# Kernel optimization log

Measured on AMD Instinct MI355X. Metric: run time of the kernel, lower is better.

## Reference

```python
import jax, jax.numpy as jnp
import numpy as np

B, N, C_IN = 16, 1024, 24
EMB, OUT, HEADS = 64, 12, 2
EMBED_SIZE = 12
HID = EMB // 2
INFLATION = 25.0


def setup_inputs() -> dict:
    rng = np.random.RandomState(0)
    # binary adjacency: ~16 random out-neighbors per node + self loops
    A = np.zeros((N, N), np.float32)
    A[np.repeat(np.arange(N), 16), rng.randint(0, N, N * 16)] = 1.0
    A[np.arange(N), np.arange(N)] = 1.0
    src, dst = np.nonzero(A)  # row-major order == torch.nonzero order
    E = src.shape[0]
    key = jax.random.key(0)
    ks = iter(jax.random.split(key, 40))

    def nrm(shape, s=0.05):
        return jax.random.normal(next(ks), shape, jnp.float32) * s

    return dict(
        x=nrm((B, N, C_IN), 1.0),
        adj=jnp.asarray(A),
        edge_index=jnp.stack([jnp.asarray(src, jnp.int32), jnp.asarray(dst, jnp.int32)]),
        edge_weight=jax.random.uniform(next(ks), (E,), jnp.float32, 0.1, 1.0),
        Wq=nrm((C_IN, C_IN)), bq=jnp.zeros((C_IN,), jnp.float32),
        Wk=nrm((C_IN, C_IN)), bk=jnp.zeros((C_IN,), jnp.float32),
        Wd=nrm((2, 2, C_IN, EMB)), bd=jnp.zeros((EMB,), jnp.float32),
        c1w0=nrm((64, C_IN, 2)), c1b0=jnp.zeros((64,), jnp.float32),
        c2w0=nrm((64, 64, 2)), c2b0=jnp.zeros((64,), jnp.float32),
        dw0=nrm((64, C_IN, 1)), db0=jnp.zeros((64,), jnp.float32),
        c1w1=nrm((EMB, 64, 2)), c1b1=jnp.zeros((EMB,), jnp.float32),
        c2w1=nrm((EMB, EMB, 2)), c2b1=jnp.zeros((EMB,), jnp.float32),
        We=nrm((EMBED_SIZE, 2 * EMB)), be=jnp.zeros((EMBED_SIZE,), jnp.float32),
        Wih=nrm((3 * HID, EMBED_SIZE)), Whh=nrm((3 * HID, HID)),
        bih=jnp.zeros((3 * HID,), jnp.float32), bhh=jnp.zeros((3 * HID,), jnp.float32),
        Wdec=nrm((OUT, HID)), bdec=jnp.zeros((OUT,), jnp.float32),
    )


def _causal_conv(x, w, b, dil):
    # torch: pad both sides by p then Chomp1d(p) on the right == left-pad only
    p = (w.shape[-1] - 1) * dil
    y = jax.lax.conv_general_dilated(x, w, (1,), [(p, 0)], rhs_dilation=(dil,),
                                     dimension_numbers=('NCH', 'OIH', 'NCH'))
    return y + b[None, :, None]


def _forward(x, adj, edge_index, edge_weight, Wq, bq, Wk, bk, Wd, bd,
             c1w0, c1b0, c2w0, c2b0, dw0, db0, c1w1, c1b1, c2w1, c2b1,
             We, be, Wih, Whh, bih, bhh, Wdec, bdec):
    src, dst = edge_index[0], edge_index[1]
    hd = C_IN // HEADS
    # --- MultiheadAttention: only averaged attn weights are used ---
    q = (x @ Wq.T + bq).reshape(B, N, HEADS, hd).transpose(0, 2, 1, 3)
    k = (x @ Wk.T + bk).reshape(B, N, HEADS, hd).transpose(0, 2, 1, 3)
    attn = jax.nn.softmax(jnp.einsum('bhqd,bhkd->bhqk', q, k) / float(np.sqrt(hd)), axis=-1)
    attn = attn.mean(axis=1)  # (B,N,N) average over heads (torch default)
    mean_w = jnp.mean(adj[None] * attn, axis=0)  # (N,N)
    # torch.nonzero(Mean_weight) == adjacency support (softmax > 0), row-major
    att_score = mean_w[src, dst]  # (E,)
    ew = INFLATION * edge_weight * att_score
    # --- DConv K=2 (torch_geometric_temporal): weighted degrees, norm*x_j messages ---
    deg_out = jnp.zeros((N,), x.dtype).at[src].add(ew)
    deg_in = jnp.zeros((N,), x.dtype).at[dst].add(ew)
    inv_out = 1.0 / deg_out
    inv_in = 1.0 / deg_in
    t1o = jnp.zeros_like(x).at[:, dst].add(x[:, src] * inv_out[src][None, :, None])
    t1i = jnp.zeros_like(x).at[:, src].add(x[:, dst] * inv_in[dst][None, :, None])
    spatial = x @ Wd[0, 0] + x @ Wd[1, 0] + t1o @ Wd[0, 1] + t1i @ Wd[1, 1] + bd
    spatial = jax.nn.relu(spatial)  # (B,N,EMB)
    # --- TCN over the node axis (x.permute(0,2,1)), dropout=identity (eval) ---
    h = x.transpose(0, 2, 1)  # (B,C,N)
    o = jax.nn.relu(_causal_conv(h, c1w0, c1b0, 1))
    o = jax.nn.relu(_causal_conv(o, c2w0, c2b0, 1))
    h = jax.nn.relu(o + _causal_conv(h, dw0, db0, 1))  # block0: downsample 1x1
    o = jax.nn.relu(_causal_conv(h, c1w1, c1b1, 2))
    o = jax.nn.relu(_causal_conv(o, c2w1, c2b1, 2))
    h = jax.nn.relu(o + h)  # block1: identity residual
    temporal = jax.nn.relu(h.transpose(0, 2, 1))  # (B,N,EMB)
    # --- fuse + embed + GRU decoder ---
    emb = jnp.concatenate([temporal, spatial], axis=-1) @ We.T + be  # (B,N,12)
    xp = emb @ Wih.T + bih  # (B,N,3H) precomputed input projections

    def step(hprev, xt):
        gh = hprev @ Whh.T + bhh
        xr, xz, xn = jnp.split(xt, 3, axis=-1)
        hr, hz, hn = jnp.split(gh, 3, axis=-1)
        r = jax.nn.sigmoid(xr + hr)
        z = jax.nn.sigmoid(xz + hz)
        n = jnp.tanh(xn + r * hn)
        hnew = (1.0 - z) * n + z * hprev
        return hnew, hnew

    _, hs = jax.lax.scan(step, jnp.zeros((B, HID), x.dtype), xp.transpose(1, 0, 2))
    hfeat = jax.nn.relu(hs.transpose(1, 0, 2))  # (B,N,HID)
    return hfeat @ Wdec.T + bdec  # (B,N,OUT)


def reference(x, adj, edge_index, edge_weight, Wq, bq, Wk, bk, Wd, bd,
              c1w0, c1b0, c2w0, c2b0, dw0, db0, c1w1, c1b1, c2w1, c2b1,
              We, be, Wih, Whh, bih, bhh, Wdec, bdec):
    return _forward(x, adj, edge_index, edge_weight, Wq, bq, Wk, bk, Wd, bd,
                    c1w0, c1b0, c2w0, c2b0, dw0, db0, c1w1, c1b1, c2w1, c2b1,
                    We, be, Wih, Whh, bih, bhh, Wdec, bdec)
```

## Files before the change

### kernel.cpp

```cpp
#include <hip/hip_runtime.h>
#include <hip/hip_bf16.h>

#define B_ 16
#define N_ 1024
#define CIN 24
#define EMB_ 64
#define HID_ 32
#define OUT_ 12
#define BH_ 32
#define RSQRT12 0.28867513459481287f
#define L2E 1.4426950408889634f

typedef unsigned uvec2 __attribute__((ext_vector_type(2)));
typedef float f2 __attribute__((ext_vector_type(2)));

#define OFF_Q2     0
#define OFF_K1     393216
#define OFF_K2     786432
#define OFF_M      1179648
#define OFF_ZI     1212416
#define OFF_DEG    1245184
#define OFF_INT    1247232
#define OFF_TEMP   1271296
#define OFF_WFT    2319872
#define OFF_BF     2332160
#define OFF_XP     2332288

__global__ __launch_bounds__(1024) void qk_prep_kernel(
    const float* __restrict__ x, const float* __restrict__ Wq, const float* __restrict__ bq,
    const float* __restrict__ Wk, const float* __restrict__ bk,
    float* __restrict__ q2, float* __restrict__ k1, float* __restrict__ k2,
    const int* __restrict__ ei, int E,
    float* __restrict__ deg, int* __restrict__ rp, int* __restrict__ cp,
    int* __restrict__ eids,
    const float* __restrict__ We, const float* __restrict__ be,
    const float* __restrict__ Wih, const float* __restrict__ bih,
    float* __restrict__ WfT, float* __restrict__ bf) {
  __shared__ int cntL[1024];
  __shared__ int sL[1024];
  __shared__ int offL[1024];
  int tid = threadIdx.x;
  if (blockIdx.x == 0) {
    deg[tid] = 0.f; deg[N_ + tid] = 0.f;
    cntL[tid] = 0;
    { int lo = 0, hi2 = E;
      while (lo < hi2) { int mid = (lo + hi2) >> 1; if (ei[mid] < tid) lo = mid + 1; else hi2 = mid; }
      rp[tid] = lo; }
    if (tid == 0) rp[N_] = E;
    __syncthreads();
    for (int e = tid; e < E; e += 1024) atomicAdd(&cntL[ei[E + e]], 1);
    __syncthreads();
    int my = cntL[tid];
    sL[tid] = my;
    __syncthreads();
    for (int d = 1; d < 1024; d <<= 1) {
      int v = (tid >= d) ? sL[tid - d] : 0;
      __syncthreads();
      sL[tid] += v;
      __syncthreads();
    }
    int excl = sL[tid] - my;
    cp[tid] = excl;
    offL[tid] = excl;
    if (tid == 1023) cp[1024] = sL[tid];
    __syncthreads();
    for (int e = tid; e < E; e += 1024) {
      int p = atomicAdd(&offL[ei[E + e]], 1);
      eids[p] = e;
    }
    for (int i = tid; i < 128 * 96; i += 1024) {
      int o = i % 96, c = i / 96;
      float acc = 0.f;
#pragma unroll
      for (int e = 0; e < 12; e++) acc += Wih[o * 12 + e] * We[e * 128 + c];
      WfT[c * 96 + o] = acc * ((o < 64) ? L2E : 2.f * L2E);
    }
    if (tid < 96) {
      float acc = bih[tid];
#pragma unroll
      for (int e = 0; e < 12; e++) acc += Wih[tid * 12 + e] * be[e];
      bf[tid] = acc * ((tid < 64) ? L2E : 2.f * L2E);
    }
  } else {
    int t = (blockIdx.x - 1) * 1024 + tid;
    int bi = t / CIN, c = t % CIN;
    int b = bi >> 10, i = bi & (N_ - 1);
    const float* xr = x + bi * CIN;
    float aq = bq[c], ak = bk[c];
#pragma unroll
    for (int d = 0; d < CIN; d++) {
      float xv = xr[d];
      aq += xv * Wq[c * CIN + d];
      ak += xv * Wk[c * CIN + d];
    }
    int h = c / 12, cc = c - h * 12;
    int bh2 = b * 2 + h;
    q2[(i * 32 + bh2) * 12 + cc] = aq;
    k1[(bh2 * N_ + i) * 12 + cc] = ak;
    k2[(i * 32 + bh2) * 12 + cc] = ak;
  }
}

#define TW 72
__global__ __launch_bounds__(512) void lse_tcn_kernel(
    const float* __restrict__ q2, const float* __restrict__ k1,
    float* __restrict__ mrow2, float* __restrict__ zinv2,
    const float* __restrict__ x,
    const float* __restrict__ c1w0, const float* __restrict__ c1b0,
    const float* __restrict__ c2w0, const float* __restrict__ c2b0,
    const float* __restrict__ dw0, const float* __restrict__ db0,
    const float* __restrict__ c1w1, const float* __restrict__ c1b1,
    const float* __restrict__ c2w1, const float* __restrict__ c2b1,
    float* __restrict__ temporal) {
  __shared__ __align__(16) char smem[53248];
  int tid = threadIdx.x;
  if (blockIdx.x < 512) {
    float* ks = (float*)smem;
    float (*pm)[64] = (float(*)[64])(smem + 49152);
    float (*pz)[64] = (float(*)[64])(smem + 51200);
    int bh = blockIdx.x >> 4;
    int rg = blockIdx.x & 15;
    const float4* k4 = (const float4*)(k1 + bh * N_ * 12);
    float4* ks4 = (float4*)ks;
    for (int i = tid; i < N_ * 3; i += 512) ks4[i] = k4[i];
    int wave = tid >> 6, lane = tid & 63;
    int row = rg * 64 + lane;
    float qr[12];
    const float* qp = q2 + ((size_t)row * 32 + bh) * 12;
#pragma unroll
    for (int c = 0; c < 12; c++) qr[c] = qp[c];
    __syncthreads();
    const float4* ksr = (const float4*)ks;
    float mloc = -1e30f, zloc = 0.f;
    for (int j = wave * 128; j < wave * 128 + 128; j++) {
      float4 k0 = ksr[j * 3], k1v = ksr[j * 3 + 1], k2v = ksr[j * 3 + 2];
      float s = qr[0] * k0.x + qr[1] * k0.y + qr[2] * k0.z + qr[3] * k0.w
              + qr[4] * k1v.x + qr[5] * k1v.y + qr[6] * k1v.z + qr[7] * k1v.w
              + qr[8] * k2v.x + qr[9] * k2v.y + qr[10] * k2v.z + qr[11] * k2v.w;
      s *= RSQRT12;
      float mn = fmaxf(mloc, s);
      zloc = zloc * __expf(mloc - mn) + __expf(s - mn);
      mloc = mn;
    }
    pm[wave][lane] = mloc;
    pz[wave][lane] = zloc;
    __syncthreads();
    if (tid < 64) {
      float M = pm[0][tid];
#pragma unroll
      for (int w2 = 1; w2 < 8; w2++) M = fmaxf(M, pm[w2][tid]);
      float Z = 0.f;
#pragma unroll
      for (int w2 = 0; w2 < 8; w2++) Z += pz[w2][tid] * __expf(pm[w2][tid] - M);
      int node = rg * 64 + tid;
      mrow2[node * 32 + bh] = M;
      zinv2[node * 32 + bh] = 1.f / Z;
    }
  } else {
    float* xs   = (float*)smem;
    float* bufA = xs + CIN * TW;
    float* bufB = bufA + 64 * TW;
    int tb = blockIdx.x - 512;
    int b = tb >> 4;
    int t0 = (tb & 15) << 6;
    int co = tid & 63, g = tid >> 6;
    for (int i = tid; i < CIN * TW; i += 512) {
      int ln = i / CIN, c = i % CIN;
      int n = t0 - 6 + ln;
      xs[c * TW + ln] = (n >= 0 && n < N_) ? x[(b * N_ + n) * CIN + c] : 0.f;
    }
    __syncthreads();
    {
      int lbase = 1 + g * 9;
      float acc[9];
      float bias = c1b0[co];
#pragma unroll
      for (int kk = 0; kk < 9; kk++) acc[kk] = bias;
      const float* wrow = c1w0 + co * 48;
      for (int ci = 0; ci < 24; ci++) {
        float w0 = wrow[ci * 2], w1 = wrow[ci * 2 + 1];
        const float* in = xs + ci * TW + lbase;
        float prev = in[-1];
#pragma unroll
        for (int kk = 0; kk < 9; kk++) { float cur = in[kk]; acc[kk] += w0 * prev + w1 * cur; prev = cur; }
      }
#pragma unroll
      for (int kk = 0; kk < 9; kk++) {
        int ln = lbase + kk;
        if (ln < TW) { int n = t0 - 6 + ln; bufB[co * TW + ln] = (n >= 0) ? fmaxf(acc[kk], 0.f) : 0.f; }
      }
    }
    __syncthreads();
    {
      int lbase = 2 + g * 9;
      float acc[9], ds[9];
      float bias = c2b0[co], dbias = db0[co];
#pragma unroll
      for (int kk = 0; kk < 9; kk++) { acc[kk] = bias; ds[kk] = dbias; }
      const float* wrow = c2w0 + co * 128;
      for (int ci = 0; ci < 64; ci++) {
        float w0 = wrow[ci * 2], w1 = wrow[ci * 2 + 1];
        const float* in = bufB + ci * TW + lbase;
        float prev = in[-1];
#pragma unroll
        for (int kk = 0; kk < 9; kk++) { float cur = in[kk]; acc[kk] += w0 * prev + w1 * cur; prev = cur; }
      }
      const float* wd = dw0 + co * 24;
      for (int ci = 0; ci < 24; ci++) {
        float wv = wd[ci];
        const float* in = xs + ci * TW + lbase;
#pragma unroll
        for (int kk = 0; kk < 9; kk++) ds[kk] += wv * in[kk];
      }
#pragma unroll
      for (int kk = 0; kk < 9; kk++) {
        int ln = lbase + kk;
        if (ln < TW) {
          int n = t0 - 6 + ln;
          float v = fmaxf(fmaxf(acc[kk], 0.f) + ds[kk], 0.f);
          bufA[co * TW + ln] = (n >= 0) ? v : 0.f;
        }
      }
    }
    __syncthreads();
    {
      int lbase = 4 + g * 9;
      float acc[9];
      float bias = c1b1[co];
#pragma unroll
      for (int kk = 0; kk < 9; kk++) acc[kk] = bias;
      const float* wrow = c1w1 + co * 128;
      for (int ci = 0; ci < 64; ci++) {
        float w0 = wrow[ci * 2], w1 = wrow[ci * 2 + 1];
        const float* in = bufA + ci * TW + lbase;
        float p2 = in[-2], p1 = in[-1];
#pragma unroll
        for (int kk = 0; kk < 9; kk++) { float cur = in[kk]; acc[kk] += w0 * p2 + w1 * cur; p2 = p1; p1 = cur; }
      }
#pragma unroll
      for (int kk = 0; kk < 9; kk++) {
        int ln = lbase + kk;
        if (ln < TW) { int n = t0 - 6 + ln; bufB[co * TW + ln] = (n >= 0) ? fmaxf(acc[kk], 0.f) : 0.f; }
      }
    }
    __syncthreads();
    {
      int lbase = 6 + g * 8;
      float acc[8];
      float bias = c2b1[co];
#pragma unroll
      for (int kk = 0; kk < 8; kk++) acc[kk] = bias;
      const float* wrow = c2w1 + co * 128;
      for (int ci = 0; ci < 64; ci++) {
        float w0 = wrow[ci * 2], w1 = wrow[ci * 2 + 1];
        const float* in = bufB + ci * TW + lbase;
        float p2 = in[-2], p1 = in[-1];
#pragma unroll
        for (int kk = 0; kk < 8; kk++) { float cur = in[kk]; acc[kk] += w0 * p2 + w1 * cur; p2 = p1; p1 = cur; }
      }
#pragma unroll
      for (int kk = 0; kk < 8; kk++) {
        int ln = lbase + kk;
        float v = fmaxf(fmaxf(acc[kk], 0.f) + bufA[co * TW + ln], 0.f);
        temporal[(b * N_ + t0 + ln - 6) * 64 + co] = v;
      }
    }
  }
}

__global__ __launch_bounds__(256) void edge_stats_kernel(
    const float* __restrict__ q2, const float* __restrict__ k2,
    const float* __restrict__ mrow2, const float* __restrict__ zinv2,
    const int* __restrict__ ei, const float* __restrict__ ewt, int E,
    float* __restrict__ deg) {
  int t = blockIdx.x * 256 + threadIdx.x;
  int e = t >> 5, bh = t & 31;
  if (e >= E) return;
  int src = ei[e], dst = ei[E + e];
  const float4* qp = (const float4*)(q2 + ((size_t)src * 32 + bh) * 12);
  const float4* kp = (const float4*)(k2 + ((size_t)dst * 32 + bh) * 12);
  float s = 0.f;
#pragma unroll
  for (int c4 = 0; c4 < 3; c4++) {
    float4 qv = qp[c4], kv = kp[c4];
    s += qv.x * kv.x + qv.y * kv.y + qv.z * kv.z + qv.w * kv.w;
  }
  s *= RSQRT12;
  float a = __expf(s - mrow2[src * 32 + bh]) * zinv2[src * 32 + bh];
  a += __shfl_xor(a, 16);
  a += __shfl_xor(a, 8);
  a += __shfl_xor(a, 4);
  a += __shfl_xor(a, 2);
  a += __shfl_xor(a, 1);
  if (bh == 0) {
    float w = 25.f * ewt[e] * (a * (1.f / 32.f));
    atomicAdd(&deg[src], w);
    atomicAdd(&deg[N_ + dst], w);
  }
}

__global__ __launch_bounds__(384) void gather_io_kernel(
    const float* __restrict__ x, const int* __restrict__ ei, int E,
    const int* __restrict__ rp, const int* __restrict__ cp, const int* __restrict__ eids,
    const float* __restrict__ deg,
    float* __restrict__ t1i, float* __restrict__ t1o) {
  __shared__ int nb[96];
  __shared__ float wv[96];
  bool isOut = blockIdx.x >= N_;
  int node = isOut ? (blockIdx.x - N_) : blockIdx.x;
  int e0 = isOut ? cp[node] : rp[node];
  int e1 = isOut ? cp[node + 1] : rp[node + 1];
  int tid = threadIdx.x;
  int b = tid / 24, c = tid % 24;
  float acc = 0.f;
  for (int base = e0; base < e1; base += 96) {
    int m = min(96, e1 - base);
    if (tid < m) {
      if (isOut) {
        int e = eids[base + tid];
        int sn = ei[e];
        nb[tid] = sn;
        wv[tid] = __builtin_amdgcn_rcpf(deg[sn]);
      } else {
        int d = ei[E + base + tid];
        nb[tid] = d;
        wv[tid] = __builtin_amdgcn_rcpf(deg[N_ + d]);
      }
    }
    __syncthreads();
    for (int t = 0; t < m; t++) acc += x[(b * N_ + nb[t]) * CIN + c] * wv[t];
    __syncthreads();
  }
  float* dst = isOut ? t1o : t1i;
  dst[(b * N_ + node) * CIN + c] = acc;
}

__global__ __launch_bounds__(384) void spatxp_kernel(
    const float* __restrict__ x, const float* __restrict__ t1o, const float* __restrict__ t1i,
    const float* __restrict__ Wd, const float* __restrict__ bd,
    const float* __restrict__ temporal,
    const float* __restrict__ WfT, const float* __restrict__ bf,
    float* __restrict__ xp) {
  __shared__ float tmp_s[64 * 64];
  __shared__ float spat_s[64 * 64];
  __shared__ float xs3[3 * 64 * 24];
  int b = blockIdx.x >> 4;
  int n0 = (blockIdx.x & 15) << 6;
  int tid = threadIdx.x;
  {
    const float4* t4 = (const float4*)(temporal + (size_t)(b * N_ + n0) * 64);
    float4* d4 = (float4*)tmp_s;
    for (int i = tid; i < 1024; i += 384) d4[i] = t4[i];
    size_t base = (size_t)(b * N_ + n0) * 24;
    const float4* xsrc = (const float4*)(x + base);
    const float4* asrc = (const float4*)(t1o + base);
    const float4* bsrc = (const float4*)(t1i + base);
    float4* xd = (float4*)xs3;
    xd[tid] = xsrc[tid];
    xd[384 + tid] = asrc[tid];
    xd[768 + tid] = bsrc[tid];
  }
  __syncthreads();
  for (int idx = tid; idx < 4096; idx += 384) {
    int nl = idx >> 6, o = idx & 63;
    const float* xr = xs3 + nl * 24;
    const float* ar = xs3 + 1536 + nl * 24;
    const float* br = xs3 + 3072 + nl * 24;
    float acc = bd[o];
#pragma unroll
    for (int d = 0; d < CIN; d++) {
      acc += xr[d] * (Wd[d * 64 + o] + Wd[3072 + d * 64 + o]);
      acc += ar[d] * Wd[1536 + d * 64 + o];
      acc += br[d] * Wd[4608 + d * 64 + o];
    }
    spat_s[nl * 64 + o] = fmaxf(acc, 0.f);
  }
  __syncthreads();
  {
    int g = tid / 96, o = tid - g * 96;
    float acc[16];
#pragma unroll
    for (int kk = 0; kk < 16; kk++) acc[kk] = bf[o];
    const float* tr = tmp_s + g * 16 * 64;
    const float* sr = spat_s + g * 16 * 64;
    for (int c = 0; c < 64; c++) {
      float w1 = WfT[c * 96 + o];
      float w2 = WfT[(64 + c) * 96 + o];
#pragma unroll
      for (int kk = 0; kk < 16; kk++) {
        acc[kk] = fmaf(tr[kk * 64 + c], w1, fmaf(sr[kk * 64 + c], w2, acc[kk]));
      }
    }
#pragma unroll
    for (int kk = 0; kk < 16; kk++)
      xp[(size_t)(b * N_ + n0 + g * 16 + kk) * 96 + o] = acc[kk];
  }
}

#define CHUNK 64
__global__ __launch_bounds__(256) void gru_kernel(
    const float* __restrict__ xp, const float* __restrict__ Whh,
    const float* __restrict__ bhh, const float* __restrict__ Wdec,
    const float* __restrict__ bdec, float* __restrict__ out) {
  __shared__ float xbuf[2][CHUNK * 96];
  __shared__ float hbuf[2][CHUNK * 36];
  __shared__ float wdec_s[12 * 36];
  __shared__ float bdec_s[12];
  int b = blockIdx.x, tid = threadIdx.x;
  int wave = tid >> 6, j = tid & 63, jl = j & 31, hi = j >> 5;
  const float* xpb = xp + (size_t)b * N_ * 96;
  {
    const float4* s4 = (const float4*)xpb;
    float4* d4 = (float4*)xbuf[0];
    for (int i = tid; i < CHUNK * 24; i += 256) d4[i] = s4[i];
    if (tid < 12) bdec_s[tid] = bdec[tid];
    for (int i = tid; i < 384; i += 256) wdec_s[(i >> 5) * 36 + (i & 31)] = Wdec[i];
  }
  f2 wA2[16], wB2[16];
  float bA = 0.f, bB = 0.f, hloc = 0.f;
  int xoff = hi ? (32 + jl) : jl;
  if (wave == 0) {
    int rowA = hi ? (32 + jl) : jl;
#pragma unroll
    for (int i = 0; i < 16; i++) {
      wA2[i] = f2{L2E * Whh[rowA * 32 + 2 * i], L2E * Whh[rowA * 32 + 2 * i + 1]};
      wB2[i] = f2{2.f * L2E * Whh[(64 + jl) * 32 + 2 * i], 2.f * L2E * Whh[(64 + jl) * 32 + 2 * i + 1]};
    }
    bA = L2E * bhh[rowA];
    bB = 2.f * L2E * bhh[64 + jl];
  }
  float4 hv4[8];
#pragma unroll
  for (int i = 0; i < 8; i++) hv4[i] = float4{0.f, 0.f, 0.f, 0.f};
  __syncthreads();
  for (int c = 0; c < 16; c++) {
    if (wave == 0) {
      const float* buf = xbuf[c & 1];
      float* hb = hbuf[c & 1];
      float xga = buf[xoff] + bA;
      float xnv = buf[64 + jl];
      for (int ln = 0; ln < CHUNK; ln++) {
        float nxga = 0.f, nxnv = 0.f;
        if (ln + 1 < CHUNK) {
          nxga = buf[(ln + 1) * 96 + xoff] + bA;
          nxnv = buf[(ln + 1) * 96 + 64 + jl];
        }
        f2 aA0 = f2{xga, 0.f}, aA1 = f2{0.f, 0.f}, aA2 = f2{0.f, 0.f}, aA3 = f2{0.f, 0.f};
        f2 aB0 = f2{bB, 0.f},  aB1 = f2{0.f, 0.f}, aB2 = f2{0.f, 0.f}, aB3 = f2{0.f, 0.f};
#pragma unroll
        for (int i = 0; i < 8; i += 2) {
          f2 h01a = f2{hv4[i].x, hv4[i].y};
          f2 h23a = f2{hv4[i].z, hv4[i].w};
          f2 h01b = f2{hv4[i + 1].x, hv4[i + 1].y};
          f2 h23b = f2{hv4[i + 1].z, hv4[i + 1].w};
          aA0 = __builtin_elementwise_fma(wA2[2 * i], h01a, aA0);
          aA1 = __builtin_elementwise_fma(wA2[2 * i + 1], h23a, aA1);
          aA2 = __builtin_elementwise_fma(wA2[2 * i + 2], h01b, aA2);
          aA3 = __builtin_elementwise_fma(wA2[2 * i + 3], h23b, aA3);
          aB0 = __builtin_elementwise_fma(wB2[2 * i], h01a, aB0);
          aB1 = __builtin_elementwise_fma(wB2[2 * i + 1], h23a, aB1);
          aB2 = __builtin_elementwise_fma(wB2[2 * i + 2], h01b, aB2);
          aB3 = __builtin_elementwise_fma(wB2[2 * i + 3], h23b, aB3);
        }
        f2 rA = (aA0 + aA1) + (aA2 + aA3);
        f2 rB = (aB0 + aB1) + (aB2 + aB3);
        float gA = rA.x + rA.y;
        float gB = rB.x + rB.y;
        float sg = __builtin_amdgcn_rcpf(1.f + exp2f(-gA));
#if __has_builtin(__builtin_amdgcn_permlane32_swap)
        uvec2 sw = __builtin_amdgcn_permlane32_swap(__float_as_uint(sg), __float_as_uint(sg), false, false);
        float zv = __uint_as_float(sw.y);
#else
        float zv = __shfl_xor(sg, 32);
#endif
        float pre = fmaf(sg, gB, xnv);
        float t = exp2f(pre);
        float nn = fmaf(-2.f, __builtin_amdgcn_rcpf(t + 1.f), 1.f);
        hloc = fmaf(zv, hloc - nn, nn);
        if (j < 32) hb[ln * 36 + jl] = hloc;
        const float4* hrow = (const float4*)(hb + ln * 36);
#pragma unroll
        for (int i = 0; i < 8; i++) hv4[i] = hrow[i];
        xga = nxga; xnv = nxnv;
      }
    } else {
      int t64 = tid - 64;
      if (c + 1 < 16) {
        const float4* s4 = (const float4*)(xpb + (size_t)(c + 1) * CHUNK * 96);
        float4* d4 = (float4*)xbuf[(c + 1) & 1];
        for (int i = t64; i < CHUNK * 24; i += 192) d4[i] = s4[i];
      }
      if (c > 0) {
        const float* hb = hbuf[(c - 1) & 1];
        int n0b = (c - 1) * CHUNK;
#pragma unroll
        for (int qq = 0; qq < 4; qq++) {
          int idx = qq * 192 + t64;
          int nl = idx / 12, o = idx - nl * 12;
          const float4* h4 = (const float4*)(hb + nl * 36);
          const float4* w4 = (const float4*)(wdec_s + o * 36);
          float acc = bdec_s[o];
#pragma unroll
          for (int i = 0; i < 8; i++) {
            float4 hv = h4[i], wv = w4[i];
            acc += fmaxf(hv.x, 0.f) * wv.x + fmaxf(hv.y, 0.f) * wv.y +
                   fmaxf(hv.z, 0.f) * wv.z + fmaxf(hv.w, 0.f) * wv.w;
          }
          out[(size_t)(b * N_ + n0b + nl) * 12 + o] = acc;
        }
      }
    }
    __syncthreads();
  }
  {
    const float* hb = hbuf[1];
    int n0b = 15 * CHUNK;
#pragma unroll
    for (int qq = 0; qq < 3; qq++) {
      int idx = qq * 256 + tid;
      int nl = idx / 12, o = idx - nl * 12;
      const float4* h4 = (const float4*)(hb + nl * 36);
      const float4* w4 = (const float4*)(wdec_s + o * 36);
      float acc = bdec_s[o];
#pragma unroll
      for (int i = 0; i < 8; i++) {
        float4 hv = h4[i], wv = w4[i];
        acc += fmaxf(hv.x, 0.f) * wv.x + fmaxf(hv.y, 0.f) * wv.y +
               fmaxf(hv.z, 0.f) * wv.z + fmaxf(hv.w, 0.f) * wv.w;
      }
      out[(size_t)(b * N_ + n0b + nl) * 12 + o] = acc;
    }
  }
}

extern "C" void kernel_launch(void* const* d_in, const int* in_sizes, int n_in,
                              void* d_out, int out_size, void* d_ws, size_t ws_size,
                              hipStream_t stream) {
  const float* x    = (const float*)d_in[0];
  const int*   ei   = (const int*)d_in[2];
  const float* ewt  = (const float*)d_in[3];
  const float* Wq   = (const float*)d_in[4];
  const float* bq   = (const float*)d_in[5];
  const float* Wk   = (const float*)d_in[6];
  const float* bk   = (const float*)d_in[7];
  const float* Wd   = (const float*)d_in[8];
  const float* bd   = (const float*)d_in[9];
  const float* c1w0 = (const float*)d_in[10];
  const float* c1b0 = (const float*)d_in[11];
  const float* c2w0 = (const float*)d_in[12];
  const float* c2b0 = (const float*)d_in[13];
  const float* dw0  = (const float*)d_in[14];
  const float* db0  = (const float*)d_in[15];
  const float* c1w1 = (const float*)d_in[16];
  const float* c1b1 = (const float*)d_in[17];
  const float* c2w1 = (const float*)d_in[18];
  const float* c2b1 = (const float*)d_in[19];
  const float* We   = (const float*)d_in[20];
  const float* be   = (const float*)d_in[21];
  const float* Wih  = (const float*)d_in[22];
  const float* Whh  = (const float*)d_in[23];
  const float* bih  = (const float*)d_in[24];
  const float* bhh  = (const float*)d_in[25];
  const float* Wdec = (const float*)d_in[26];
  const float* bdec = (const float*)d_in[27];
  float* out = (float*)d_out;
  float* w = (float*)d_ws;
  const int E = in_sizes[2] / 2;

  float* q2    = w + OFF_Q2;
  float* k1    = w + OFF_K1;
  float* k2    = w + OFF_K2;
  float* mrow2 = w + OFF_M;
  float* zinv2 = w + OFF_ZI;
  float* deg   = w + OFF_DEG;
  float* t1o   = w + OFF_Q2;
  float* t1i   = w + OFF_K1;
  float* temp  = w + OFF_TEMP;
  float* WfT   = w + OFF_WFT;
  float* bf    = w + OFF_BF;
  float* xp    = w + OFF_XP;
  int* ib   = (int*)(w + OFF_INT);
  int* rp   = ib;
  int* cp   = ib + 1028;
  int* eids = ib + 2056;

  qk_prep_kernel<<<385, 1024, 0, stream>>>(x, Wq, bq, Wk, bk, q2, k1, k2,
                                           ei, E, deg, rp, cp, eids,
                                           We, be, Wih, bih, WfT, bf);
  lse_tcn_kernel<<<768, 512, 0, stream>>>(q2, k1, mrow2, zinv2, x,
                                          c1w0, c1b0, c2w0, c2b0, dw0, db0,
                                          c1w1, c1b1, c2w1, c2b1, temp);
  edge_stats_kernel<<<(E * 32 + 255) / 256, 256, 0, stream>>>(q2, k2, mrow2, zinv2, ei, ewt, E, deg);
  gather_io_kernel<<<2 * N_, 384, 0, stream>>>(x, ei, E, rp, cp, eids, deg, t1i, t1o);
  spatxp_kernel<<<B_ * 16, 384, 0, stream>>>(x, t1o, t1i, Wd, bd, temp, WfT, bf, xp);
  gru_kernel<<<B_, 256, 0, stream>>>(xp, Whh, bhh, Wdec, bdec, out);
}
```

Measured before the change: 380.6 us.

## Regroup kernels: merge TCN into prep, fuse neighbor gather into spatxp, simplify GRU FMA chain

Moves the TCN work out of the LSE kernel into the prep/QK-projection kernel, now launched with 512-thread blocks, so the TCN overlaps with the graph preprocessing. LSE becomes its own kernel. The separate gather_io kernel is removed and its in/out neighbor aggregation is computed inside spatxp into shared memory, which saves one launch and a global round trip. The GRU matvec also switches from four independent accumulators to a single dependent FMA chain, which lengthens latency on the serial recurrence. Doing the gather inside spatxp puts it on only 256 blocks, giving less parallelism than the 2048-block gather kernel had.

```diff
diff --git a/kernel.cpp b/kernel.cpp
--- a/kernel.cpp
+++ b/kernel.cpp
@@ -26,7 +26,9 @@
 #define OFF_BF     2332160
 #define OFF_XP     2332288
 
-__global__ __launch_bounds__(1024) void qk_prep_kernel(
+#define TW 72
+
+__global__ __launch_bounds__(512) void prep_tcn_qk_kernel(
     const float* __restrict__ x, const float* __restrict__ Wq, const float* __restrict__ bq,
     const float* __restrict__ Wk, const float* __restrict__ bk,
     float* __restrict__ q2, float* __restrict__ k1, float* __restrict__ k2,
@@ -35,77 +37,7 @@
     int* __restrict__ eids,
     const float* __restrict__ We, const float* __restrict__ be,
     const float* __restrict__ Wih, const float* __restrict__ bih,
-    float* __restrict__ WfT, float* __restrict__ bf) {
-  __shared__ int cntL[1024];
-  __shared__ int sL[1024];
-  __shared__ int offL[1024];
-  int tid = threadIdx.x;
-  if (blockIdx.x == 0) {
-    deg[tid] = 0.f; deg[N_ + tid] = 0.f;
-    cntL[tid] = 0;
-    { int lo = 0, hi2 = E;
-      while (lo < hi2) { int mid = (lo + hi2) >> 1; if (ei[mid] < tid) lo = mid + 1; else hi2 = mid; }
-      rp[tid] = lo; }
-    if (tid == 0) rp[N_] = E;
-    __syncthreads();
-    for (int e = tid; e < E; e += 1024) atomicAdd(&cntL[ei[E + e]], 1);
-    __syncthreads();
-    int my = cntL[tid];
-    sL[tid] = my;
-    __syncthreads();
-    for (int d = 1; d < 1024; d <<= 1) {
-      int v = (tid >= d) ? sL[tid - d] : 0;
-      __syncthreads();
-      sL[tid] += v;
-      __syncthreads();
-    }
-    int excl = sL[tid] - my;
-    cp[tid] = excl;
-    offL[tid] = excl;
-    if (tid == 1023) cp[1024] = sL[tid];
-    __syncthreads();
-    for (int e = tid; e < E; e += 1024) {
-      int p = atomicAdd(&offL[ei[E + e]], 1);
-      eids[p] = e;
-    }
-    for (int i = tid; i < 128 * 96; i += 1024) {
-      int o = i % 96, c = i / 96;
-      float acc = 0.f;
-#pragma unroll
-      for (int e = 0; e < 12; e++) acc += Wih[o * 12 + e] * We[e * 128 + c];
-      WfT[c * 96 + o] = acc * ((o < 64) ? L2E : 2.f * L2E);
-    }
-    if (tid < 96) {
-      float acc = bih[tid];
-#pragma unroll
-      for (int e = 0; e < 12; e++) acc += Wih[tid * 12 + e] * be[e];
-      bf[tid] = acc * ((tid < 64) ? L2E : 2.f * L2E);
-    }
-  } else {
-    int t = (blockIdx.x - 1) * 1024 + tid;
-    int bi = t / CIN, c = t % CIN;
-    int b = bi >> 10, i = bi & (N_ - 1);
-    const float* xr = x + bi * CIN;
-    float aq = bq[c], ak = bk[c];
-#pragma unroll
-    for (int d = 0; d < CIN; d++) {
-      float xv = xr[d];
-      aq += xv * Wq[c * CIN + d];
-      ak += xv * Wk[c * CIN + d];
-    }
-    int h = c / 12, cc = c - h * 12;
-    int bh2 = b * 2 + h;
-    q2[(i * 32 + bh2) * 12 + cc] = aq;
-    k1[(bh2 * N_ + i) * 12 + cc] = ak;
-    k2[(i * 32 + bh2) * 12 + cc] = ak;
-  }
-}
-
-#define TW 72
-__global__ __launch_bounds__(512) void lse_tcn_kernel(
-    const float* __restrict__ q2, const float* __restrict__ k1,
-    float* __restrict__ mrow2, float* __restrict__ zinv2,
-    const float* __restrict__ x,
+    float* __restrict__ WfT, float* __restrict__ bf,
     const float* __restrict__ c1w0, const float* __restrict__ c1b0,
     const float* __restrict__ c2w0, const float* __restrict__ c2b0,
     const float* __restrict__ dw0, const float* __restrict__ db0,
@@ -114,53 +46,61 @@
     float* __restrict__ temporal) {
   __shared__ __align__(16) char smem[53248];
   int tid = threadIdx.x;
-  if (blockIdx.x < 512) {
-    float* ks = (float*)smem;
-    float (*pm)[64] = (float(*)[64])(smem + 49152);
-    float (*pz)[64] = (float(*)[64])(smem + 51200);
-    int bh = blockIdx.x >> 4;
-    int rg = blockIdx.x & 15;
-    const float4* k4 = (const float4*)(k1 + bh * N_ * 12);
-    float4* ks4 = (float4*)ks;
-    for (int i = tid; i < N_ * 3; i += 512) ks4[i] = k4[i];
-    int wave = tid >> 6, lane = tid & 63;
-    int row = rg * 64 + lane;
-    float qr[12];
-    const float* qp = q2 + ((size_t)row * 32 + bh) * 12;
-#pragma unroll
-    for (int c = 0; c < 12; c++) qr[c] = qp[c];
-    __syncthreads();
-    const float4* ksr = (const float4*)ks;
-    float mloc = -1e30f, zloc = 0.f;
-    for (int j = wave * 128; j < wave * 128 + 128; j++) {
-      float4 k0 = ksr[j * 3], k1v = ksr[j * 3 + 1], k2v = ksr[j * 3 + 2];
-      float s = qr[0] * k0.x + qr[1] * k0.y + qr[2] * k0.z + qr[3] * k0.w
-              + qr[4] * k1v.x + qr[5] * k1v.y + qr[6] * k1v.z + qr[7] * k1v.w
-              + qr[8] * k2v.x + qr[9] * k2v.y + qr[10] * k2v.z + qr[11] * k2v.w;
-      s *= RSQRT12;
-      float mn = fmaxf(mloc, s);
-      zloc = zloc * __expf(mloc - mn) + __expf(s - mn);
-      mloc = mn;
-    }
-    pm[wave][lane] = mloc;
-    pz[wave][lane] = zloc;
-    __syncthreads();
-    if (tid < 64) {
-      float M = pm[0][tid];
-#pragma unroll
-      for (int w2 = 1; w2 < 8; w2++) M = fmaxf(M, pm[w2][tid]);
-      float Z = 0.f;
-#pragma unroll
-      for (int w2 = 0; w2 < 8; w2++) Z += pz[w2][tid] * __expf(pm[w2][tid] - M);
-      int node = rg * 64 + tid;
-      mrow2[node * 32 + bh] = M;
-      zinv2[node * 32 + bh] = 1.f / Z;
-    }
-  } else {
+  if (blockIdx.x == 0) {
+    int* cntL = (int*)smem;
+    int* sL   = (int*)(smem + 4096);
+    int* offL = (int*)(smem + 8192);
+    for (int i = tid; i < 2 * N_; i += 512) deg[i] = 0.f;
+    cntL[tid] = 0; cntL[tid + 512] = 0;
+#pragma unroll
+    for (int ii = 0; ii < 2; ii++) {
+      int i = tid + ii * 512;
+      int lo = 0, hi2 = E;
+      while (lo < hi2) { int mid = (lo + hi2) >> 1; if (ei[mid] < i) lo = mid + 1; else hi2 = mid; }
+      rp[i] = lo;
+    }
+    if (tid == 0) rp[N_] = E;
+    __syncthreads();
+    for (int e = tid; e < E; e += 512) atomicAdd(&cntL[ei[E + e]], 1);
+    __syncthreads();
+    int my0 = cntL[tid], my1 = cntL[tid + 512];
+    sL[tid] = my0; sL[tid + 512] = my1;
+    __syncthreads();
+    for (int d = 1; d < 1024; d <<= 1) {
+      int v0 = (tid >= d) ? sL[tid - d] : 0;
+      int i1 = tid + 512;
+      int v1 = sL[i1 - d];
+      __syncthreads();
+      sL[tid] += v0; sL[i1] += v1;
+      __syncthreads();
+    }
+    int ex0 = sL[tid] - my0, ex1 = sL[tid + 512] - my1;
+    cp[tid] = ex0; cp[tid + 512] = ex1;
+    offL[tid] = ex0; offL[tid + 512] = ex1;
+    if (tid == 511) cp[1024] = sL[1023];
+    __syncthreads();
+    for (int e = tid; e < E; e += 512) {
+      int p = atomicAdd(&offL[ei[E + e]], 1);
+      eids[p] = e;
+    }
+    for (int i = tid; i < 128 * 96; i += 512) {
+      int o = i % 96, c = i / 96;
+      float acc = 0.f;
+#pragma unroll
+      for (int e = 0; e < 12; e++) acc += Wih[o * 12 + e] * We[e * 128 + c];
+      WfT[c * 96 + o] = acc * ((o < 64) ? L2E : 2.f * L2E);
+    }
+    if (tid < 96) {
+      float acc = bih[tid];
+#pragma unroll
+      for (int e = 0; e < 12; e++) acc += Wih[tid * 12 + e] * be[e];
+      bf[tid] = acc * ((tid < 64) ? L2E : 2.f * L2E);
+    }
+  } else if (blockIdx.x <= 256) {
     float* xs   = (float*)smem;
     float* bufA = xs + CIN * TW;
     float* bufB = bufA + 64 * TW;
-    int tb = blockIdx.x - 512;
+    int tb = blockIdx.x - 1;
     int b = tb >> 4;
     int t0 = (tb & 15) << 6;
     int co = tid & 63, g = tid >> 6;
@@ -265,6 +205,71 @@
         temporal[(b * N_ + t0 + ln - 6) * 64 + co] = v;
       }
     }
+  } else {
+    int t = (blockIdx.x - 257) * 512 + tid;
+    int bi = t / CIN, c = t % CIN;
+    int b = bi >> 10, i = bi & (N_ - 1);
+    const float* xr = x + bi * CIN;
+    float aq = bq[c], ak = bk[c];
+#pragma unroll
+    for (int d = 0; d < CIN; d++) {
+      float xv = xr[d];
+      aq += xv * Wq[c * CIN + d];
+      ak += xv * Wk[c * CIN + d];
+    }
+    int h = c / 12, cc = c - h * 12;
+    int bh2 = b * 2 + h;
+    q2[(i * 32 + bh2) * 12 + cc] = aq;
+    k1[(bh2 * N_ + i) * 12 + cc] = ak;
+    k2[(i * 32 + bh2) * 12 + cc] = ak;
+  }
+}
+
+__global__ __launch_bounds__(512) void lse_kernel(
+    const float* __restrict__ q2, const float* __restrict__ k1,
+    float* __restrict__ mrow2, float* __restrict__ zinv2) {
+  __shared__ __align__(16) char smem[53248];
+  int tid = threadIdx.x;
+  float* ks = (float*)smem;
+  float (*pm)[64] = (float(*)[64])(smem + 49152);
+  float (*pz)[64] = (float(*)[64])(smem + 51200);
+  int bh = blockIdx.x >> 4;
+  int rg = blockIdx.x & 15;
+  const float4* k4 = (const float4*)(k1 + bh * N_ * 12);
+  float4* ks4 = (float4*)ks;
+  for (int i = tid; i < N_ * 3; i += 512) ks4[i] = k4[i];
+  int wave = tid >> 6, lane = tid & 63;
+  int row = rg * 64 + lane;
+  float qr[12];
+  const float* qp = q2 + ((size_t)row * 32 + bh) * 12;
+#pragma unroll
+  for (int c = 0; c < 12; c++) qr[c] = qp[c];
+  __syncthreads();
+  const float4* ksr = (const float4*)ks;
+  float mloc = -1e30f, zloc = 0.f;
+  for (int j = wave * 128; j < wave * 128 + 128; j++) {
+    float4 k0 = ksr[j * 3], k1v = ksr[j * 3 + 1], k2v = ksr[j * 3 + 2];
+    float s = qr[0] * k0.x + qr[1] * k0.y + qr[2] * k0.z + qr[3] * k0.w
+            + qr[4] * k1v.x + qr[5] * k1v.y + qr[6] * k1v.z + qr[7] * k1v.w
+            + qr[8] * k2v.x + qr[9] * k2v.y + qr[10] * k2v.z + qr[11] * k2v.w;
+    s *= RSQRT12;
+    float mn = fmaxf(mloc, s);
+    zloc = zloc * __expf(mloc - mn) + __expf(s - mn);
+    mloc = mn;
+  }
+  pm[wave][lane] = mloc;
+  pz[wave][lane] = zloc;
+  __syncthreads();
+  if (tid < 64) {
+    float M = pm[0][tid];
+#pragma unroll
+    for (int w2 = 1; w2 < 8; w2++) M = fmaxf(M, pm[w2][tid]);
+    float Z = 0.f;
+#pragma unroll
+    for (int w2 = 0; w2 < 8; w2++) Z += pz[w2][tid] * __expf(pm[w2][tid] - M);
+    int node = rg * 64 + tid;
+    mrow2[node * 32 + bh] = M;
+    zinv2[node * 32 + bh] = 1.f / Z;
   }
 }
 
@@ -299,51 +304,20 @@
   }
 }
 
-__global__ __launch_bounds__(384) void gather_io_kernel(
-    const float* __restrict__ x, const int* __restrict__ ei, int E,
+__global__ __launch_bounds__(384) void spatxp_kernel(
+    const float* __restrict__ x,
+    const int* __restrict__ ei, int E,
     const int* __restrict__ rp, const int* __restrict__ cp, const int* __restrict__ eids,
     const float* __restrict__ deg,
-    float* __restrict__ t1i, float* __restrict__ t1o) {
-  __shared__ int nb[96];
-  __shared__ float wv[96];
-  bool isOut = blockIdx.x >= N_;
-  int node = isOut ? (blockIdx.x - N_) : blockIdx.x;
-  int e0 = isOut ? cp[node] : rp[node];
-  int e1 = isOut ? cp[node + 1] : rp[node + 1];
-  int tid = threadIdx.x;
-  int b = tid / 24, c = tid % 24;
-  float acc = 0.f;
-  for (int base = e0; base < e1; base += 96) {
-    int m = min(96, e1 - base);
-    if (tid < m) {
-      if (isOut) {
-        int e = eids[base + tid];
-        int sn = ei[e];
-        nb[tid] = sn;
-        wv[tid] = __builtin_amdgcn_rcpf(deg[sn]);
-      } else {
-        int d = ei[E + base + tid];
-        nb[tid] = d;
-        wv[tid] = __builtin_amdgcn_rcpf(deg[N_ + d]);
-      }
-    }
-    __syncthreads();
-    for (int t = 0; t < m; t++) acc += x[(b * N_ + nb[t]) * CIN + c] * wv[t];
-    __syncthreads();
-  }
-  float* dst = isOut ? t1o : t1i;
-  dst[(b * N_ + node) * CIN + c] = acc;
-}
-
-__global__ __launch_bounds__(384) void spatxp_kernel(
-    const float* __restrict__ x, const float* __restrict__ t1o, const float* __restrict__ t1i,
     const float* __restrict__ Wd, const float* __restrict__ bd,
     const float* __restrict__ temporal,
     const float* __restrict__ WfT, const float* __restrict__ bf,
     float* __restrict__ xp) {
   __shared__ float tmp_s[64 * 64];
   __shared__ float spat_s[64 * 64];
-  __shared__ float xs3[3 * 64 * 24];
+  __shared__ float xs[64 * 24];
+  __shared__ float t1i_s[64 * 24];
+  __shared__ float t1o_s[64 * 24];
   int b = blockIdx.x >> 4;
   int n0 = (blockIdx.x & 15) << 6;
   int tid = threadIdx.x;
@@ -351,21 +325,34 @@
     const float4* t4 = (const float4*)(temporal + (size_t)(b * N_ + n0) * 64);
     float4* d4 = (float4*)tmp_s;
     for (int i = tid; i < 1024; i += 384) d4[i] = t4[i];
-    size_t base = (size_t)(b * N_ + n0) * 24;
-    const float4* xsrc = (const float4*)(x + base);
-    const float4* asrc = (const float4*)(t1o + base);
-    const float4* bsrc = (const float4*)(t1i + base);
-    float4* xd = (float4*)xs3;
-    xd[tid] = xsrc[tid];
-    xd[384 + tid] = asrc[tid];
-    xd[768 + tid] = bsrc[tid];
+    const float4* xsrc = (const float4*)(x + (size_t)(b * N_ + n0) * 24);
+    ((float4*)xs)[tid] = xsrc[tid];
+  }
+  for (int idx = tid; idx < 1536; idx += 384) {
+    int nl = idx / 24, c = idx - nl * 24;
+    int node = n0 + nl;
+    float acci = 0.f;
+    int e0 = rp[node], e1 = rp[node + 1];
+    for (int e = e0; e < e1; e++) {
+      int nb = ei[E + e];
+      acci += x[(size_t)(b * N_ + nb) * 24 + c] * __builtin_amdgcn_rcpf(deg[N_ + nb]);
+    }
+    t1i_s[nl * 24 + c] = acci;
+    float acco = 0.f;
+    int p0 = cp[node], p1 = cp[node + 1];
+    for (int p = p0; p < p1; p++) {
+      int e2 = eids[p];
+      int sn = ei[e2];
+      acco += x[(size_t)(b * N_ + sn) * 24 + c] * __builtin_amdgcn_rcpf(deg[sn]);
+    }
+    t1o_s[nl * 24 + c] = acco;
   }
   __syncthreads();
   for (int idx = tid; idx < 4096; idx += 384) {
     int nl = idx >> 6, o = idx & 63;
-    const float* xr = xs3 + nl * 24;
-    const float* ar = xs3 + 1536 + nl * 24;
-    const float* br = xs3 + 3072 + nl * 24;
+    const float* xr = xs + nl * 24;
+    const float* ar = t1o_s + nl * 24;
+    const float* br = t1i_s + nl * 24;
     float acc = bd[o];
 #pragma unroll
     for (int d = 0; d < CIN; d++) {
@@ -445,27 +432,19 @@
           nxga = buf[(ln + 1) * 96 + xoff] + bA;
           nxnv = buf[(ln + 1) * 96 + 64 + jl];
         }
-        f2 aA0 = f2{xga, 0.f}, aA1 = f2{0.f, 0.f}, aA2 = f2{0.f, 0.f}, aA3 = f2{0.f, 0.f};
-        f2 aB0 = f2{bB, 0.f},  aB1 = f2{0.f, 0.f}, aB2 = f2{0.f, 0.f}, aB3 = f2{0.f, 0.f};
-#pragma unroll
-        for (int i = 0; i < 8; i += 2) {
-          f2 h01a = f2{hv4[i].x, hv4[i].y};
-          f2 h23a = f2{hv4[i].z, hv4[i].w};
-          f2 h01b = f2{hv4[i + 1].x, hv4[i + 1].y};
-          f2 h23b = f2{hv4[i + 1].z, hv4[i + 1].w};
-          aA0 = __builtin_elementwise_fma(wA2[2 * i], h01a, aA0);
-          aA1 = __builtin_elementwise_fma(wA2[2 * i + 1], h23a, aA1);
-          aA2 = __builtin_elementwise_fma(wA2[2 * i + 2], h01b, aA2);
-          aA3 = __builtin_elementwise_fma(wA2[2 * i + 3], h23b, aA3);
-          aB0 = __builtin_elementwise_fma(wB2[2 * i], h01a, aB0);
-          aB1 = __builtin_elementwise_fma(wB2[2 * i + 1], h23a, aB1);
-          aB2 = __builtin_elementwise_fma(wB2[2 * i + 2], h01b, aB2);
-          aB3 = __builtin_elementwise_fma(wB2[2 * i + 3], h23b, aB3);
+        f2 aA = f2{xga, 0.f};
+        f2 aB = f2{bB, 0.f};
+#pragma unroll
+        for (int i = 0; i < 8; i++) {
+          f2 h01 = f2{hv4[i].x, hv4[i].y};
+          f2 h23 = f2{hv4[i].z, hv4[i].w};
+          aA = __builtin_elementwise_fma(wA2[2 * i], h01, aA);
+          aB = __builtin_elementwise_fma(wB2[2 * i], h01, aB);
+          aA = __builtin_elementwise_fma(wA2[2 * i + 1], h23, aA);
+          aB = __builtin_elementwise_fma(wB2[2 * i + 1], h23, aB);
         }
-        f2 rA = (aA0 + aA1) + (aA2 + aA3);
-        f2 rB = (aB0 + aB1) + (aB2 + aB3);
-        float gA = rA.x + rA.y;
-        float gB = rB.x + rB.y;
+        float gA = aA.x + aA.y;
+        float gB = aB.x + aB.y;
         float sg = __builtin_amdgcn_rcpf(1.f + exp2f(-gA));
 #if __has_builtin(__builtin_amdgcn_permlane32_swap)
         uvec2 sw = __builtin_amdgcn_permlane32_swap(__float_as_uint(sg), __float_as_uint(sg), false, false);
@@ -573,8 +552,6 @@
   float* mrow2 = w + OFF_M;
   float* zinv2 = w + OFF_ZI;
   float* deg   = w + OFF_DEG;
-  float* t1o   = w + OFF_Q2;
-  float* t1i   = w + OFF_K1;
   float* temp  = w + OFF_TEMP;
   float* WfT   = w + OFF_WFT;
   float* bf    = w + OFF_BF;
@@ -584,14 +561,14 @@
   int* cp   = ib + 1028;
   int* eids = ib + 2056;
 
-  qk_prep_kernel<<<385, 1024, 0, stream>>>(x, Wq, bq, Wk, bk, q2, k1, k2,
-                                           ei, E, deg, rp, cp, eids,
-                                           We, be, Wih, bih, WfT, bf);
-  lse_tcn_kernel<<<768, 512, 0, stream>>>(q2, k1, mrow2, zinv2, x,
-                                          c1w0, c1b0, c2w0, c2b0, dw0, db0,
-                                          c1w1, c1b1, c2w1, c2b1, temp);
+  prep_tcn_qk_kernel<<<1025, 512, 0, stream>>>(x, Wq, bq, Wk, bk, q2, k1, k2,
+                                               ei, E, deg, rp, cp, eids,
+                                               We, be, Wih, bih, WfT, bf,
+                                               c1w0, c1b0, c2w0, c2b0, dw0, db0,
+                                               c1w1, c1b1, c2w1, c2b1, temp);
+  lse_kernel<<<512, 512, 0, stream>>>(q2, k1, mrow2, zinv2);
   edge_stats_kernel<<<(E * 32 + 255) / 256, 256, 0, stream>>>(q2, k2, mrow2, zinv2, ei, ewt, E, deg);
-  gather_io_kernel<<<2 * N_, 384, 0, stream>>>(x, ei, E, rp, cp, eids, deg, t1i, t1o);
-  spatxp_kernel<<<B_ * 16, 384, 0, stream>>>(x, t1o, t1i, Wd, bd, temp, WfT, bf, xp);
+  spatxp_kernel<<<B_ * 16, 384, 0, stream>>>(x, ei, E, rp, cp, eids, deg,
+                                             Wd, bd, temp, WfT, bf, xp);
   gru_kernel<<<B_, 256, 0, stream>>>(xp, Whh, bhh, Wdec, bdec, out);
 }
```

After: 406.0 us. 6.7% more time.
